# Kernel tuning notes

Measured on AMD Instinct MI355X. Metric: run time of the kernel, lower is better.

Reference implementation:

```python
import jax, jax.numpy as jnp
import numpy as np
from math import sqrt

D = 512        # output_dim (layer_dims[-1])
H = 4          # num_heads
ATN = D // H   # atn_dim = 128
BERT_D = 768
B = 32         # number of graph pairs
NP = 4096
NH = 4096


def setup_inputs() -> dict:
    key = jax.random.key(0)
    ks = jax.random.split(key, 20)
    inp = {
        'ctx_p': jax.random.normal(ks[0], (NP, D), jnp.float32),
        'ctx_h': jax.random.normal(ks[1], (NH, D), jnp.float32),
        'lhs_p': jax.random.normal(ks[2], (NP, BERT_D), jnp.float32),
        'lhs_h': jax.random.normal(ks[3], (NH, BERT_D), jnp.float32),
        'batch_p': jnp.sort(jax.random.randint(ks[4], (NP,), 0, B)).astype(jnp.int64),
        'batch_h': jnp.sort(jax.random.randint(ks[5], (NH,), 0, B)).astype(jnp.int64),
        # learned parameters (stored [in, out])
        'Wq': jax.random.normal(ks[6], (D, D), jnp.float32) * 0.02,
        'bq': jnp.zeros((D,), jnp.float32),
        'Wk': jax.random.normal(ks[7], (D, D), jnp.float32) * 0.02,
        'bk': jnp.zeros((D,), jnp.float32),
        'Wv': jax.random.normal(ks[8], (BERT_D, BERT_D), jnp.float32) * 0.02,
        'bv': jnp.zeros((BERT_D,), jnp.float32),
        'W1': jax.random.normal(ks[9], (D + BERT_D, 256), jnp.float32) * 0.02,
        'b1': jnp.zeros((256,), jnp.float32),
        'W2': jax.random.normal(ks[10], (256, 128), jnp.float32) * 0.02,
        'ln_g': jnp.ones((128,), jnp.float32),
        'ln_b': jnp.zeros((128,), jnp.float32),
        'Wc': jax.random.normal(ks[11], (128, 3), jnp.float32) * 0.02,
        'bc': jnp.zeros((3,), jnp.float32),
    }
    return inp


def reference(ctx_p, ctx_h, lhs_p, lhs_h, batch_p, batch_h,
              Wq, bq, Wk, bk, Wv, bv, W1, b1, W2, ln_g, ln_b, Wc, bc):
    # q/k projections; torch code does .view(-1, atn_dim, num_heads) -> head is fastest axis
    qs = (ctx_h @ Wq + bq).reshape(-1, ATN, H)          # [nh, atn, H]
    ks = (ctx_p @ Wk + bk).reshape(-1, ATN, H)          # [np, atn, H]
    vs = (lhs_p @ Wv + bv).reshape(-1, H, BERT_D // H)  # [np, H, 768/H]

    atn = jnp.einsum('ndh,mdh->nmh', qs, ks) / sqrt(ATN)  # [nh, np, H]
    # faithful to original: positions where batch ids MATCH are set to -1e10
    mask_same = batch_h[:, None] == batch_p[None, :]       # [nh, np]
    atn = jnp.where(mask_same[:, :, None], jnp.float32(-1e10), atn)
    atn = jax.nn.softmax(atn, axis=1)                      # softmax over premise words m

    attended = jnp.einsum('nmh,mhd->nhd', atn, vs).reshape(-1, BERT_D)  # [nh, 768]

    feats = jnp.concatenate([ctx_h, lhs_h - attended], axis=1)  # [nh, D+768]
    h1 = jax.nn.gelu(feats @ W1 + b1, approximate=False)
    h2 = h1 @ W2                                                # Linear no bias
    mu = h2.mean(axis=-1, keepdims=True)
    var = ((h2 - mu) ** 2).mean(axis=-1, keepdims=True)
    h2 = (h2 - mu) * jax.lax.rsqrt(var + 1e-5) * ln_g + ln_b    # LayerNorm(128)

    # global_mean_pool over batch_h
    pooled = jax.ops.segment_sum(h2, batch_h, num_segments=B)
    counts = jax.ops.segment_sum(jnp.ones((h2.shape[0], 1), h2.dtype), batch_h, num_segments=B)
    pooled = pooled / jnp.maximum(counts, 1.0)

    return pooled @ Wc + bc  # [B, 3]
```

## Files before the change

kernel.cpp:

```cpp
#include <hip/hip_runtime.h>
#include <hip/hip_bf16.h>
#include <math.h>

#define NP_N 4096
#define NH_N 4096
#define D_N 512
#define BERT_N 768
#define H_N 4
#define B_N 32
#define SCL2 0.12754245006257576f

typedef __attribute__((ext_vector_type(8))) short short8;
typedef __attribute__((ext_vector_type(4))) float f32x4;
typedef __attribute__((ext_vector_type(4))) unsigned short ush4;
typedef __attribute__((ext_vector_type(4))) unsigned int uivec4;
typedef unsigned short ushort_t;

__device__ __forceinline__ void gl_lds16(const void* g, void* l) {
    __builtin_amdgcn_global_load_lds((const __attribute__((address_space(1))) void*)g,
                                     (__attribute__((address_space(3))) void*)l, 16, 0, 0);
}
__device__ __forceinline__ unsigned short f2bu(float f) {
    __hip_bfloat16 b = __float2bfloat16(f);
    return *reinterpret_cast<unsigned short*>(&b);
}
__device__ __forceinline__ float b2f(unsigned short u) {
    union { unsigned int i; float f; } x; x.i = ((unsigned int)u) << 16; return x.f;
}
__device__ __forceinline__ unsigned int pkbf(float a, float b) {
    union { __hip_bfloat162 h; unsigned int u; } x;
    x.h.x = __float2bfloat16(a);
    x.h.y = __float2bfloat16(b);
    return x.u;
}
__device__ __forceinline__ unsigned int sxor(unsigned int v, int m) {
    return (unsigned int)__shfl_xor((int)v, m);
}

__device__ __forceinline__ short8 mkfrag(uint2 u, uint2 v, bool hi, bool godd) {
    unsigned ux32 = sxor(u.x, 32), uy32 = sxor(u.y, 32);
    unsigned vx32 = sxor(v.x, 32), vy32 = sxor(v.y, 32);
    unsigned ax = hi ? vx32 : u.x, bx = hi ? v.x : ux32;
    unsigned ay = hi ? vy32 : u.y, by = hi ? v.y : uy32;
    unsigned sbx = sxor(bx, 16), sax = sxor(ax, 16);
    unsigned sby = sxor(by, 16), say = sxor(ay, 16);
    uivec4 w;
    w.x = godd ? sbx : ax;
    w.y = godd ? sby : ay;
    w.z = godd ? bx : sax;
    w.w = godd ? by : say;
    return __builtin_bit_cast(short8, w);
}

__global__ __launch_bounds__(256) void convert_all(
    const float* __restrict__ ctx_h, const float* __restrict__ ctx_p,
    const float* __restrict__ lhs_p,
    const float* __restrict__ Wq, const float* __restrict__ Wk,
    const float* __restrict__ Wv, const float* __restrict__ W1,
    const float* __restrict__ bq, const float* __restrict__ bk,
    ushort_t* __restrict__ ctxp_bf, ushort_t* __restrict__ lhsp_bf,
    ushort_t* __restrict__ feats,
    ushort_t* __restrict__ Wqt, ushort_t* __restrict__ Wkt,
    ushort_t* __restrict__ Wvt, ushort_t* __restrict__ W1t,
    float* __restrict__ bqp, float* __restrict__ bkp)
{
    const int bid = blockIdx.x, t = threadIdx.x;
    if (bid < 128) {
        for (long k = (long)bid * 256 + t; k < 524288; k += 128 * 256) {
            float4 v = ((const float4*)ctx_h)[k];
            ush4 o; o[0] = f2bu(v.x); o[1] = f2bu(v.y); o[2] = f2bu(v.z); o[3] = f2bu(v.w);
            long n = k >> 7, c4 = k & 127;
            ((ush4*)feats)[n * 320 + c4] = o;
        }
        if (bid == 0) {
            for (int n = t; n < 512; n += 256) {
                int np = (n & 3) * 128 + (n >> 2);
                bqp[np] = bq[n] * SCL2;
                bkp[np] = bk[n];
            }
        }
        return;
    }
    if (bid < 256) {
        for (long k = (long)(bid - 128) * 256 + t; k < 524288; k += 128 * 256) {
            float4 v = ((const float4*)ctx_p)[k];
            ush4 o; o[0] = f2bu(v.x); o[1] = f2bu(v.y); o[2] = f2bu(v.z); o[3] = f2bu(v.w);
            ((ush4*)ctxp_bf)[k] = o;
        }
        return;
    }
    if (bid < 448) {
        for (long k = (long)(bid - 256) * 256 + t; k < 786432; k += 192 * 256) {
            float4 v = ((const float4*)lhs_p)[k];
            ush4 o; o[0] = f2bu(v.x); o[1] = f2bu(v.y); o[2] = f2bu(v.z); o[3] = f2bu(v.w);
            ((ush4*)lhsp_bf)[k] = o;
        }
        return;
    }
    int tb = bid - 448;
    const float* src; ushort_t* dst; int K, N, tile, perm; float wscl;
    if (tb < 64)       { src = Wq; dst = Wqt; K = 512;  N = 512; tile = tb;       perm = 1; wscl = SCL2; }
    else if (tb < 128) { src = Wk; dst = Wkt; K = 512;  N = 512; tile = tb - 64;  perm = 1; wscl = 1.f; }
    else if (tb < 272) { src = Wv; dst = Wvt; K = 768;  N = 768; tile = tb - 128; perm = 0; wscl = 1.f; }
    else               { src = W1; dst = W1t; K = 1280; N = 256; tile = tb - 272; perm = 0; wscl = 1.f; }
    int ntn = N >> 6;
    int k0 = (tile / ntn) * 64, n0 = (tile % ntn) * 64;
    __shared__ float tl[64][65];
#pragma unroll
    for (int i = 0; i < 16; i++) {
        int idx = t + i * 256; int r = idx >> 6, c = idx & 63;
        tl[r][c] = src[(size_t)(k0 + r) * N + n0 + c];
    }
    __syncthreads();
#pragma unroll
    for (int i = 0; i < 16; i++) {
        int idx = t + i * 256; int r = idx >> 6, c = idx & 63;
        int n = n0 + r;
        int nr = perm ? ((n & 3) * 128 + (n >> 2)) : n;
        dst[(size_t)nr * K + k0 + c] = f2bu(tl[c][r] * wscl);
    }
}

__global__ __launch_bounds__(256) void gemm_qkv(
    const ushort_t* __restrict__ feats, const ushort_t* __restrict__ ctxp,
    const ushort_t* __restrict__ Wqt, const ushort_t* __restrict__ Wkt,
    const ushort_t* __restrict__ Wvt, const ushort_t* __restrict__ lhsp,
    const float* __restrict__ bqp, const float* __restrict__ bkp,
    const float* __restrict__ bv,
    ushort_t* __restrict__ Qb, ushort_t* __restrict__ Kb,
    ushort_t* __restrict__ Vtb)
{
    int b = blockIdx.x;
    const ushort_t *A, *Bt; const float* bias; ushort_t* C;
    int lda, N, K, m0, n0, bias_row;
    if (b < 512) {
        A = feats; lda = 1280; Bt = Wqt; bias = bqp; C = Qb;
        N = 512; K = 512; bias_row = 0;
        n0 = (b & 7) * 64; m0 = (b >> 3) * 64;
    } else if (b < 1024) {
        b -= 512;
        A = ctxp; lda = 512; Bt = Wkt; bias = bkp; C = Kb;
        N = 512; K = 512; bias_row = 0;
        n0 = (b & 7) * 64; m0 = (b >> 3) * 64;
    } else {
        b -= 1024;
        A = Wvt; lda = 768; Bt = lhsp; bias = bv; C = Vtb;
        N = 4096; K = 768; bias_row = 1;
        n0 = (b & 63) * 64; m0 = (b >> 6) * 64;
    }
    const int nsteps = K >> 6;

    __shared__ ushort_t As[2][64 * 64];
    __shared__ ushort_t Bs[2][64 * 64];
    const int t = threadIdx.x, w = t >> 6, lane = t & 63;
    const int lq = lane & 15, g = lane >> 4;
    const int wm = w >> 1, wn = w & 1;

    f32x4 acc[2][2] = {};

    auto STAGE = [&](int buf, int k0) {
#pragma unroll
        for (int jj = 0; jj < 2; jj++) {
            int j = w * 2 + jj;
            int r = j * 8 + (lane >> 3);
            int c = ((lane & 7) * 16) ^ ((r & 7) << 4);
            gl_lds16((const char*)A + ((size_t)(m0 + r) * lda + k0) * 2 + c,
                     (void*)&As[buf][j * 512]);
            gl_lds16((const char*)Bt + ((size_t)(n0 + r) * K + k0) * 2 + c,
                     (void*)&Bs[buf][j * 512]);
        }
    };

    STAGE(0, 0);
    __syncthreads();
    int cur = 0;
    for (int s = 0; s < nsteps; s++) {
        if (s + 1 < nsteps) STAGE(cur ^ 1, (s + 1) * 64);
        const char* Ab = (const char*)&As[cur][0];
        const char* Bb = (const char*)&Bs[cur][0];
        const int swz = (lq & 7) << 4;
        short8 af[2][2], bfr[2][2];
#pragma unroll
        for (int mf = 0; mf < 2; mf++) {
            int r = wm * 32 + mf * 16 + lq;
#pragma unroll
            for (int ks = 0; ks < 2; ks++)
                af[mf][ks] = *(const short8*)(Ab + r * 128 + ((ks * 64 + g * 16) ^ swz));
        }
#pragma unroll
        for (int nf = 0; nf < 2; nf++) {
            int r = wn * 32 + nf * 16 + lq;
#pragma unroll
            for (int ks = 0; ks < 2; ks++)
                bfr[nf][ks] = *(const short8*)(Bb + r * 128 + ((ks * 64 + g * 16) ^ swz));
        }
#pragma unroll
        for (int mf = 0; mf < 2; mf++)
#pragma unroll
            for (int nf = 0; nf < 2; nf++)
#pragma unroll
                for (int ks = 0; ks < 2; ks++)
                    acc[mf][nf] = __builtin_amdgcn_mfma_f32_16x16x32_bf16(
                        af[mf][ks], bfr[nf][ks], acc[mf][nf], 0, 0, 0);
        __syncthreads();
        cur ^= 1;
    }

#pragma unroll
    for (int mf = 0; mf < 2; mf++) {
#pragma unroll
        for (int nf = 0; nf < 2; nf++) {
            int ncol = n0 + wn * 32 + nf * 16 + lq;
            float bcol = bias_row ? 0.f : bias[ncol];
#pragma unroll
            for (int j = 0; j < 4; j++) {
                int mrow = m0 + wm * 32 + mf * 16 + 4 * g + j;
                float v = acc[mf][nf][j] + (bias_row ? bias[mrow] : bcol);
                C[(size_t)mrow * N + ncol] = f2bu(v);
            }
        }
    }
}

__global__ __launch_bounds__(256) void gemm_mlp1(
    const ushort_t* __restrict__ A, int lda, const ushort_t* __restrict__ Bt,
    const float* __restrict__ bias, ushort_t* __restrict__ C,
    int M, int N, int K)
{
    __shared__ ushort_t As[2][64 * 64];
    __shared__ ushort_t Bs[2][64 * 64];
    const int t = threadIdx.x, w = t >> 6, lane = t & 63;
    const int lq = lane & 15, g = lane >> 4;
    const int wm = w >> 1, wn = w & 1;
    const int n0 = blockIdx.x * 64, m0 = blockIdx.y * 64;
    const int nsteps = K >> 6;

    f32x4 acc[2][2] = {};

    auto STAGE = [&](int buf, int k0) {
#pragma unroll
        for (int jj = 0; jj < 2; jj++) {
            int j = w * 2 + jj;
            int r = j * 8 + (lane >> 3);
            int c = ((lane & 7) * 16) ^ ((r & 7) << 4);
            gl_lds16((const char*)A + ((size_t)(m0 + r) * lda + k0) * 2 + c,
                     (void*)&As[buf][j * 512]);
            gl_lds16((const char*)Bt + ((size_t)(n0 + r) * K + k0) * 2 + c,
                     (void*)&Bs[buf][j * 512]);
        }
    };

    STAGE(0, 0);
    __syncthreads();
    int cur = 0;
    for (int s = 0; s < nsteps; s++) {
        if (s + 1 < nsteps) STAGE(cur ^ 1, (s + 1) * 64);
        const char* Ab = (const char*)&As[cur][0];
        const char* Bb = (const char*)&Bs[cur][0];
        const int swz = (lq & 7) << 4;
        short8 af[2][2], bfr[2][2];
#pragma unroll
        for (int mf = 0; mf < 2; mf++) {
            int r = wm * 32 + mf * 16 + lq;
#pragma unroll
            for (int ks = 0; ks < 2; ks++)
                af[mf][ks] = *(const short8*)(Ab + r * 128 + ((ks * 64 + g * 16) ^ swz));
        }
#pragma unroll
        for (int nf = 0; nf < 2; nf++) {
            int r = wn * 32 + nf * 16 + lq;
#pragma unroll
            for (int ks = 0; ks < 2; ks++)
                bfr[nf][ks] = *(const short8*)(Bb + r * 128 + ((ks * 64 + g * 16) ^ swz));
        }
#pragma unroll
        for (int mf = 0; mf < 2; mf++)
#pragma unroll
            for (int nf = 0; nf < 2; nf++)
#pragma unroll
                for (int ks = 0; ks < 2; ks++)
                    acc[mf][nf] = __builtin_amdgcn_mfma_f32_16x16x32_bf16(
                        af[mf][ks], bfr[nf][ks], acc[mf][nf], 0, 0, 0);
        __syncthreads();
        cur ^= 1;
    }

#pragma unroll
    for (int mf = 0; mf < 2; mf++) {
#pragma unroll
        for (int nf = 0; nf < 2; nf++) {
            int ncol = n0 + wn * 32 + nf * 16 + lq;
            float bcol = bias[ncol];
#pragma unroll
            for (int j = 0; j < 4; j++) {
                int mrow = m0 + wm * 32 + mf * 16 + 4 * g + j;
                float v = acc[mf][nf][j] + bcol;
                v = 0.5f * v * (1.f + erff(v * 0.70710678118654752f));
                C[(size_t)mrow * N + ncol] = f2bu(v);
            }
        }
    }
}

__global__ __launch_bounds__(256, 2) void attn_mfma(
    const ushort_t* __restrict__ Qb,
    const ushort_t* __restrict__ Kb,
    const ushort_t* __restrict__ Vtb,
    const int* __restrict__ batch_h, const int* __restrict__ batch_p,
    ushort_t* __restrict__ Opart,
    float* __restrict__ lsums)
{
    const int bid = blockIdx.x;
    const int h = (bid & 7) >> 1;
    const int outer = bid & 1;
    const int n0 = (bid >> 3) * 64;

    __shared__ __align__(16) char smem[81920];

    const int t = threadIdx.x;
    const int w = t >> 6;
    const int qc = w & 1;
    const int st = w >> 1;
    const int lane = t & 63, lq = lane & 15, g = lane >> 4;
    const int lqm = (lq & 7) << 4;
    const bool hi = lane >= 32;
    const bool godd = (lane & 16) != 0;

    char* base = smem + st * 40960;
    char* Kt0 = base;
    char* Kt1 = base + 8192;
    char* Vt0 = base + 16384;
    char* Vt1 = base + 28672;

    short8 qf[2][4];
    int bhq[2];
#pragma unroll
    for (int qg = 0; qg < 2; qg++) {
        const ushort_t* qrow = Qb + (size_t)(n0 + qc * 32 + qg * 16 + lq) * 512 + h * 128;
#pragma unroll
        for (int ks = 0; ks < 4; ks++)
            qf[qg][ks] = *(const short8*)(qrow + ks * 32 + g * 8);
        bhq[qg] = batch_h[n0 + qc * 32 + qg * 16 + lq];
    }

    f32x4 Ofr[2][12];
#pragma unroll
    for (int qg = 0; qg < 2; qg++)
#pragma unroll
        for (int nt = 0; nt < 12; nt++) Ofr[qg][nt] = (f32x4){0.f, 0.f, 0.f, 0.f};
    float l_run[2] = {0.f, 0.f};

    const char* Kg = (const char*)Kb;
    const char* Vg = (const char*)Vtb;
    const int kb = outer * 2048 + st * 1024;

    const int voff = ((lq >> 1) * 128) + ((((lq & 1) * 64) + g * 16) ^ (((lq >> 1) & 7) << 4));

    auto STAGE = [&](char* Kd, char* Vd, int m0k) {
#pragma unroll
        for (int jj = 0; jj < 4; jj++) {
            int j = qc * 4 + jj;
            int r = j * 4 + (lane >> 4);
            int c = ((lane & 15) * 16) ^ ((r & 7) << 4);
            gl_lds16(Kg + (size_t)(m0k + r) * 1024 + h * 256 + c, Kd + j * 1024);
        }
#pragma unroll
        for (int jj = 0; jj < 6; jj++) {
            int j = qc * 6 + jj;
            int rp = j * 8 + (lane >> 3);
            int inner = ((lane & 7) * 16) ^ ((rp & 7) << 4);
            int vd = rp * 2 + (inner >> 6);
            int kby = inner & 63;
            gl_lds16(Vg + ((size_t)(h * 192 + vd) * 4096 + m0k) * 2 + kby, Vd + j * 1024);
        }
    };

    STAGE(Kt0, Vt0, kb);
    asm volatile("s_waitcnt vmcnt(0)" ::: "memory");
    __builtin_amdgcn_s_barrier();
    int cur = 0;

    for (int tile = 0; tile < 32; tile++) {
        char* Kc = cur ? Kt1 : Kt0;
        char* Vc = cur ? Vt1 : Vt0;
        const int ktb = kb + tile * 32;

        int4 bp0 = *(const int4*)&batch_p[ktb + 4 * g];
        int4 bp1 = *(const int4*)&batch_p[ktb + 16 + 4 * g];

        if (tile + 1 < 32) STAGE(cur ? Kt0 : Kt1, cur ? Vt0 : Vt1, ktb + 32);

        f32x4 S[2][2];
#pragma unroll
        for (int qg = 0; qg < 2; qg++)
#pragma unroll
            for (int mt = 0; mt < 2; mt++) S[qg][mt] = (f32x4){0.f, 0.f, 0.f, 0.f};
        __builtin_amdgcn_s_setprio(1);
#pragma unroll
        for (int mt = 0; mt < 2; mt++) {
            const char* rbase = Kc + (mt * 16 + lq) * 256;
#pragma unroll
            for (int ks = 0; ks < 4; ks++) {
                short8 kf = *(const short8*)(rbase + ((ks * 64 + g * 16) ^ lqm));
                S[0][mt] = __builtin_amdgcn_mfma_f32_16x16x32_bf16(kf, qf[0][ks], S[0][mt], 0, 0, 0);
                S[1][mt] = __builtin_amdgcn_mfma_f32_16x16x32_bf16(kf, qf[1][ks], S[1][mt], 0, 0, 0);
            }
        }
        __builtin_amdgcn_s_setprio(0);

        uint2 P2[2][2];
#pragma unroll
        for (int qg = 0; qg < 2; qg++) {
            float e0 = (bp0.x == bhq[qg]) ? 0.f : exp2f(S[qg][0][0]);
            float e1 = (bp0.y == bhq[qg]) ? 0.f : exp2f(S[qg][0][1]);
            float e2 = (bp0.z == bhq[qg]) ? 0.f : exp2f(S[qg][0][2]);
            float e3 = (bp0.w == bhq[qg]) ? 0.f : exp2f(S[qg][0][3]);
            float f0 = (bp1.x == bhq[qg]) ? 0.f : exp2f(S[qg][1][0]);
            float f1 = (bp1.y == bhq[qg]) ? 0.f : exp2f(S[qg][1][1]);
            float f2 = (bp1.z == bhq[qg]) ? 0.f : exp2f(S[qg][1][2]);
            float f3 = (bp1.w == bhq[qg]) ? 0.f : exp2f(S[qg][1][3]);
            l_run[qg] += ((e0 + e1) + (e2 + e3)) + ((f0 + f1) + (f2 + f3));
            P2[qg][0].x = pkbf(e0, e1); P2[qg][0].y = pkbf(e2, e3);
            P2[qg][1].x = pkbf(f0, f1); P2[qg][1].y = pkbf(f2, f3);
        }

        short8 pf0 = mkfrag(P2[0][0], P2[0][1], hi, godd);
        short8 pf1 = mkfrag(P2[1][0], P2[1][1], hi, godd);
        __builtin_amdgcn_s_setprio(1);
#pragma unroll
        for (int nt = 0; nt < 12; nt++) {
            short8 vf = *(const short8*)(Vc + nt * 1024 + voff);
            Ofr[0][nt] = __builtin_amdgcn_mfma_f32_16x16x32_bf16(pf0, vf, Ofr[0][nt], 0, 0, 0);
            Ofr[1][nt] = __builtin_amdgcn_mfma_f32_16x16x32_bf16(pf1, vf, Ofr[1][nt], 0, 0, 0);
        }
        __builtin_amdgcn_s_setprio(0);

        asm volatile("s_waitcnt vmcnt(0)" ::: "memory");
        __builtin_amdgcn_s_barrier();
        cur ^= 1;
    }

    float lt[2];
#pragma unroll
    for (int qg = 0; qg < 2; qg++) {
        float l = l_run[qg];
        l += __shfl_xor(l, 16);
        l += __shfl_xor(l, 32);
        lt[qg] = l;
    }

    float* mO = (float*)smem;
    float* mls = (float*)(smem + 49152);
    if (st == 1) {
        float* dst = mO + ((size_t)qc * 64 + lane) * 96;
#pragma unroll
        for (int qg = 0; qg < 2; qg++) {
#pragma unroll
            for (int nt = 0; nt < 12; nt++)
                *(f32x4*)(dst + qg * 48 + nt * 4) = Ofr[qg][nt];
            if (g == 0) mls[(qc * 2 + qg) * 16 + lq] = lt[qg];
        }
    }
    __syncthreads();
    if (st == 0) {
        const float* srcO = mO + ((size_t)qc * 64 + lane) * 96;
        const size_t plane = (size_t)(outer * 4 + h) * 4096;
#pragma unroll
        for (int qg = 0; qg < 2; qg++) {
            int q0 = n0 + qc * 32 + qg * 16;
            if (g == 0)
                lsums[plane + q0 + lq] = lt[qg] + mls[(qc * 2 + qg) * 16 + lq];
#pragma unroll
            for (int nt = 0; nt < 12; nt++) {
                f32x4 o1 = *(const f32x4*)(srcO + qg * 48 + nt * 4);
#pragma unroll
                for (int j = 0; j < 4; j++)
                    Opart[(plane + q0 + 4 * g + j) * 192 + nt * 16 + lq] =
                        f2bu(Ofr[qg][nt][j] + o1[j]);
            }
        }
    }
}

__global__ __launch_bounds__(256) void combine_feats(
    const ushort_t* __restrict__ Opart, const float* __restrict__ lsums,
    const float* __restrict__ lhs_h, ushort_t* __restrict__ feats)
{
    const int t = threadIdx.x;
#pragma unroll
    for (int i = 0; i < 4; i++) {
        int q = blockIdx.x * 4 + i;
#pragma unroll
        for (int it = 0; it < 3; it++) {
            int c = t + it * 256;
            int h = c / 192, vd = c - h * 192;
            size_t i0 = (size_t)h * 4096 + q;
            size_t i1 = (size_t)(4 + h) * 4096 + q;
            float linv = 1.f / (lsums[i0] + lsums[i1]);
            float O = (b2f(Opart[i0 * 192 + vd]) + b2f(Opart[i1 * 192 + vd])) * linv;
            feats[(size_t)q * 1280 + 512 + c] = f2bu(lhs_h[(size_t)q * 768 + c] - O);
        }
    }
}

__global__ __launch_bounds__(256) void h2_ln(
    const ushort_t* __restrict__ h1, const float* __restrict__ W2,
    const float* __restrict__ ln_g, const float* __restrict__ ln_b,
    float* __restrict__ h2out)
{
    const int n0 = blockIdx.x * 8;
    const int t = threadIdx.x;
    __shared__ float h1s[8][256];
    __shared__ float h2s[8][128];

#pragma unroll
    for (int i = 0; i < 8; i++) {
        int idx = t + i * 256; int r = idx >> 8, c = idx & 255;
        h1s[r][c] = b2f(h1[(size_t)(n0 + r) * 256 + c]);
    }
    __syncthreads();

    {
        int o2 = t & 127, gq = t >> 7;
        float acc[4] = {};
        for (int k4 = 0; k4 < 64; k4++) {
            float w0 = W2[(size_t)(k4 * 4 + 0) * 128 + o2];
            float w1 = W2[(size_t)(k4 * 4 + 1) * 128 + o2];
            float w2 = W2[(size_t)(k4 * 4 + 2) * 128 + o2];
            float w3 = W2[(size_t)(k4 * 4 + 3) * 128 + o2];
#pragma unroll
            for (int q = 0; q < 4; q++) {
                float4 hh = *(const float4*)&h1s[gq * 4 + q][k4 * 4];
                acc[q] += hh.x * w0 + hh.y * w1 + hh.z * w2 + hh.w * w3;
            }
        }
#pragma unroll
        for (int q = 0; q < 4; q++) h2s[gq * 4 + q][o2] = acc[q];
    }
    __syncthreads();

    {
        int wv = t >> 6, lane = t & 63;
#pragma unroll
        for (int sx = 0; sx < 2; sx++) {
            int nd = wv * 2 + sx;
            float x0 = h2s[nd][lane], x1 = h2s[nd][lane + 64];
            float sum = x0 + x1;
#pragma unroll
            for (int off = 32; off; off >>= 1) sum += __shfl_xor(sum, off);
            float mu = sum * (1.f / 128.f);
            float d0 = x0 - mu, d1 = x1 - mu;
            float s2 = d0 * d0 + d1 * d1;
#pragma unroll
            for (int off = 32; off; off >>= 1) s2 += __shfl_xor(s2, off);
            float rstd = rsqrtf(s2 * (1.f / 128.f) + 1e-5f);
            size_t base = (size_t)(n0 + nd) * 128;
            h2out[base + lane]      = d0 * rstd * ln_g[lane] + ln_b[lane];
            h2out[base + lane + 64] = d1 * rstd * ln_g[lane + 64] + ln_b[lane + 64];
        }
    }
}

__global__ __launch_bounds__(128) void pool_cls(
    const float* __restrict__ h2, const int* __restrict__ batch_h,
    const float* __restrict__ Wc, const float* __restrict__ bc,
    float* __restrict__ out)
{
    int b = blockIdx.x, t = threadIdx.x;
    __shared__ int bounds[2];
    if (t < 2) {
        int target = b + t;
        int lo = 0, hi = NH_N;
        while (lo < hi) {
            int mid = (lo + hi) >> 1;
            if (batch_h[mid] < target) lo = mid + 1; else hi = mid;
        }
        bounds[t] = lo;
    }
    __syncthreads();
    int s = bounds[0], e = bounds[1];
    float acc = 0.f;
    for (int n = s; n < e; n++) acc += h2[(size_t)n * 128 + t];
    float pooled = acc / fmaxf((float)(e - s), 1.f);
    __shared__ float red[128];
    for (int c = 0; c < 3; c++) {
        red[t] = pooled * Wc[t * 3 + c];
        __syncthreads();
        for (int off = 64; off > 0; off >>= 1) {
            if (t < off) red[t] += red[t + off];
            __syncthreads();
        }
        if (t == 0) out[b * 3 + c] = red[0] + bc[c];
        __syncthreads();
    }
}

extern "C" void kernel_launch(void* const* d_in, const int* in_sizes, int n_in,
                              void* d_out, int out_size, void* d_ws, size_t ws_size,
                              hipStream_t stream)
{
    const float* ctx_p  = (const float*)d_in[0];
    const float* ctx_h  = (const float*)d_in[1];
    const float* lhs_p  = (const float*)d_in[2];
    const float* lhs_h  = (const float*)d_in[3];
    const int*   batch_p = (const int*)d_in[4];
    const int*   batch_h = (const int*)d_in[5];
    const float* Wq = (const float*)d_in[6];
    const float* bq = (const float*)d_in[7];
    const float* Wk = (const float*)d_in[8];
    const float* bk = (const float*)d_in[9];
    const float* Wv = (const float*)d_in[10];
    const float* bv = (const float*)d_in[11];
    const float* W1 = (const float*)d_in[12];
    const float* b1 = (const float*)d_in[13];
    const float* W2 = (const float*)d_in[14];
    const float* ln_g = (const float*)d_in[15];
    const float* ln_b = (const float*)d_in[16];
    const float* Wc = (const float*)d_in[17];
    const float* bc = (const float*)d_in[18];
    float* out = (float*)d_out;

    ushort_t* u = (ushort_t*)d_ws;
    ushort_t* ctxp_bf = u;
    ushort_t* lhsp_bf = ctxp_bf + 2097152;
    ushort_t* Wqt  = lhsp_bf + 3145728;
    ushort_t* Wkt  = Wqt + 262144;
    ushort_t* Wvt  = Wkt + 262144;
    ushort_t* Opart = u;
    ushort_t* W1t  = Wvt + 589824;
    ushort_t* Qb   = W1t + 327680;
    ushort_t* Kb   = Qb + 2097152;
    ushort_t* Vtb  = Kb + 2097152;
    ushort_t* feats = Vtb + 3145728;
    ushort_t* h1   = feats + 5242880;
    float* lsums = (float*)(h1 + 1048576);
    float* h2  = lsums + 65536;
    float* bqp = h2 + 524288;
    float* bkp = bqp + 512;

    convert_all<<<800, 256, 0, stream>>>(
        ctx_h, ctx_p, lhs_p, Wq, Wk, Wv, W1, bq, bk,
        ctxp_bf, lhsp_bf, feats, Wqt, Wkt, Wvt, W1t, bqp, bkp);

    gemm_qkv<<<1792, 256, 0, stream>>>(
        feats, ctxp_bf, Wqt, Wkt, Wvt, lhsp_bf, bqp, bkp, bv, Qb, Kb, Vtb);

    attn_mfma<<<512, 256, 0, stream>>>(Qb, Kb, Vtb, batch_h, batch_p, Opart, lsums);

    combine_feats<<<1024, 256, 0, stream>>>(Opart, lsums, lhs_h, feats);

    gemm_mlp1<<<dim3(4, 64), 256, 0, stream>>>(feats, 1280, W1t, b1, h1, NH_N, 256, 1280);

    h2_ln<<<512, 256, 0, stream>>>(h1, W2, ln_g, ln_b, h2);
    pool_cls<<<B_N, 128, 0, stream>>>(h2, batch_h, Wc, bc, out);
}
```

Before: 194.3 us.

## Use single-buffered 64-key tiles instead of double-buffered 32-key tiles in attention

The attention loop now processes 64 keys per tile with one K/V LDS buffer, replacing the double-buffered 32-key tiles. The V tile layout is simplified to row-per-d with an XOR swizzle. This halves the number of loop iterations and barriers and gives more MFMA work per tile. The cost is that global-to-LDS loads for the next tile are no longer overlapped with compute: the loop waits for them between two barriers, which exposes load latency.

```diff
diff --git a/kernel.cpp b/kernel.cpp
--- a/kernel.cpp
+++ b/kernel.cpp
@@ -327,10 +327,8 @@
     const bool godd = (lane & 16) != 0;
 
     char* base = smem + st * 40960;
-    char* Kt0 = base;
-    char* Kt1 = base + 8192;
-    char* Vt0 = base + 16384;
-    char* Vt1 = base + 28672;
+    char* Kbuf = base;
+    char* Vbuf = base + 16384;
 
     short8 qf[2][4];
     int bhq[2];
@@ -354,51 +352,44 @@
     const char* Vg = (const char*)Vtb;
     const int kb = outer * 2048 + st * 1024;
 
-    const int voff = ((lq >> 1) * 128) + ((((lq & 1) * 64) + g * 16) ^ (((lq >> 1) & 7) << 4));
-
-    auto STAGE = [&](char* Kd, char* Vd, int m0k) {
-#pragma unroll
-        for (int jj = 0; jj < 4; jj++) {
-            int j = qc * 4 + jj;
+    auto STAGE = [&](int m0k) {
+#pragma unroll
+        for (int jj = 0; jj < 8; jj++) {
+            int j = qc * 8 + jj;
             int r = j * 4 + (lane >> 4);
             int c = ((lane & 15) * 16) ^ ((r & 7) << 4);
-            gl_lds16(Kg + (size_t)(m0k + r) * 1024 + h * 256 + c, Kd + j * 1024);
-        }
-#pragma unroll
-        for (int jj = 0; jj < 6; jj++) {
-            int j = qc * 6 + jj;
-            int rp = j * 8 + (lane >> 3);
-            int inner = ((lane & 7) * 16) ^ ((rp & 7) << 4);
-            int vd = rp * 2 + (inner >> 6);
-            int kby = inner & 63;
-            gl_lds16(Vg + ((size_t)(h * 192 + vd) * 4096 + m0k) * 2 + kby, Vd + j * 1024);
+            gl_lds16(Kg + (size_t)(m0k + r) * 1024 + h * 256 + c, Kbuf + j * 1024);
+        }
+#pragma unroll
+        for (int jj = 0; jj < 12; jj++) {
+            int j = qc * 12 + jj;
+            int r = j * 8 + (lane >> 3);
+            int c = ((lane & 7) * 16) ^ ((r & 7) << 4);
+            gl_lds16(Vg + ((size_t)(h * 192 + r) * 4096 + m0k) * 2 + c, Vbuf + j * 1024);
         }
     };
 
-    STAGE(Kt0, Vt0, kb);
+    STAGE(kb);
     asm volatile("s_waitcnt vmcnt(0)" ::: "memory");
     __builtin_amdgcn_s_barrier();
-    int cur = 0;
-
-    for (int tile = 0; tile < 32; tile++) {
-        char* Kc = cur ? Kt1 : Kt0;
-        char* Vc = cur ? Vt1 : Vt0;
-        const int ktb = kb + tile * 32;
-
-        int4 bp0 = *(const int4*)&batch_p[ktb + 4 * g];
-        int4 bp1 = *(const int4*)&batch_p[ktb + 16 + 4 * g];
-
-        if (tile + 1 < 32) STAGE(cur ? Kt0 : Kt1, cur ? Vt0 : Vt1, ktb + 32);
-
-        f32x4 S[2][2];
+
+    for (int tile = 0; tile < 16; tile++) {
+        const int ktb = kb + tile * 64;
+
+        int4 bp4[4];
+#pragma unroll
+        for (int mt = 0; mt < 4; mt++)
+            bp4[mt] = *(const int4*)&batch_p[ktb + mt * 16 + 4 * g];
+
+        f32x4 S[2][4];
 #pragma unroll
         for (int qg = 0; qg < 2; qg++)
 #pragma unroll
-            for (int mt = 0; mt < 2; mt++) S[qg][mt] = (f32x4){0.f, 0.f, 0.f, 0.f};
+            for (int mt = 0; mt < 4; mt++) S[qg][mt] = (f32x4){0.f, 0.f, 0.f, 0.f};
         __builtin_amdgcn_s_setprio(1);
 #pragma unroll
-        for (int mt = 0; mt < 2; mt++) {
-            const char* rbase = Kc + (mt * 16 + lq) * 256;
+        for (int mt = 0; mt < 4; mt++) {
+            const char* rbase = Kbuf + (mt * 16 + lq) * 256;
 #pragma unroll
             for (int ks = 0; ks < 4; ks++) {
                 short8 kf = *(const short8*)(rbase + ((ks * 64 + g * 16) ^ lqm));
@@ -408,36 +399,43 @@
         }
         __builtin_amdgcn_s_setprio(0);
 
-        uint2 P2[2][2];
+        uint2 P2[2][4];
 #pragma unroll
         for (int qg = 0; qg < 2; qg++) {
-            float e0 = (bp0.x == bhq[qg]) ? 0.f : exp2f(S[qg][0][0]);
-            float e1 = (bp0.y == bhq[qg]) ? 0.f : exp2f(S[qg][0][1]);
-            float e2 = (bp0.z == bhq[qg]) ? 0.f : exp2f(S[qg][0][2]);
-            float e3 = (bp0.w == bhq[qg]) ? 0.f : exp2f(S[qg][0][3]);
-            float f0 = (bp1.x == bhq[qg]) ? 0.f : exp2f(S[qg][1][0]);
-            float f1 = (bp1.y == bhq[qg]) ? 0.f : exp2f(S[qg][1][1]);
-            float f2 = (bp1.z == bhq[qg]) ? 0.f : exp2f(S[qg][1][2]);
-            float f3 = (bp1.w == bhq[qg]) ? 0.f : exp2f(S[qg][1][3]);
-            l_run[qg] += ((e0 + e1) + (e2 + e3)) + ((f0 + f1) + (f2 + f3));
-            P2[qg][0].x = pkbf(e0, e1); P2[qg][0].y = pkbf(e2, e3);
-            P2[qg][1].x = pkbf(f0, f1); P2[qg][1].y = pkbf(f2, f3);
-        }
-
-        short8 pf0 = mkfrag(P2[0][0], P2[0][1], hi, godd);
-        short8 pf1 = mkfrag(P2[1][0], P2[1][1], hi, godd);
-        __builtin_amdgcn_s_setprio(1);
-#pragma unroll
-        for (int nt = 0; nt < 12; nt++) {
-            short8 vf = *(const short8*)(Vc + nt * 1024 + voff);
-            Ofr[0][nt] = __builtin_amdgcn_mfma_f32_16x16x32_bf16(pf0, vf, Ofr[0][nt], 0, 0, 0);
-            Ofr[1][nt] = __builtin_amdgcn_mfma_f32_16x16x32_bf16(pf1, vf, Ofr[1][nt], 0, 0, 0);
-        }
-        __builtin_amdgcn_s_setprio(0);
-
-        asm volatile("s_waitcnt vmcnt(0)" ::: "memory");
+            float lsum = 0.f;
+#pragma unroll
+            for (int mt = 0; mt < 4; mt++) {
+                float e0 = (bp4[mt].x == bhq[qg]) ? 0.f : exp2f(S[qg][mt][0]);
+                float e1 = (bp4[mt].y == bhq[qg]) ? 0.f : exp2f(S[qg][mt][1]);
+                float e2 = (bp4[mt].z == bhq[qg]) ? 0.f : exp2f(S[qg][mt][2]);
+                float e3 = (bp4[mt].w == bhq[qg]) ? 0.f : exp2f(S[qg][mt][3]);
+                lsum += (e0 + e1) + (e2 + e3);
+                P2[qg][mt].x = pkbf(e0, e1);
+                P2[qg][mt].y = pkbf(e2, e3);
+            }
+            l_run[qg] += lsum;
+        }
+
+#pragma unroll
+        for (int ks = 0; ks < 2; ks++) {
+            short8 pf0 = mkfrag(P2[0][2 * ks], P2[0][2 * ks + 1], hi, godd);
+            short8 pf1 = mkfrag(P2[1][2 * ks], P2[1][2 * ks + 1], hi, godd);
+            __builtin_amdgcn_s_setprio(1);
+#pragma unroll
+            for (int nt = 0; nt < 12; nt++) {
+                short8 vf = *(const short8*)(Vbuf + (nt * 16 + lq) * 128 + ((ks * 64 + g * 16) ^ lqm));
+                Ofr[0][nt] = __builtin_amdgcn_mfma_f32_16x16x32_bf16(pf0, vf, Ofr[0][nt], 0, 0, 0);
+                Ofr[1][nt] = __builtin_amdgcn_mfma_f32_16x16x32_bf16(pf1, vf, Ofr[1][nt], 0, 0, 0);
+            }
+            __builtin_amdgcn_s_setprio(0);
+        }
+
         __builtin_amdgcn_s_barrier();
-        cur ^= 1;
+        if (tile + 1 < 16) {
+            STAGE(ktb + 64);
+            asm volatile("s_waitcnt vmcnt(0)" ::: "memory");
+        }
+        __builtin_amdgcn_s_barrier();
     }
 
     float lt[2];
```

Measured after the change: 199.6 us. +2.8%, slower.
